# Performance work log

Measured on AMD Instinct MI355X. Metric: run time of the kernel, lower is better.

Reference implementation:

```python
import jax, jax.numpy as jnp
import numpy as np

PI = float(np.pi)          # ouro.pi_center
THIRD = 2.0 * PI / 3.0     # ouro.third_offset
EPB = PI                   # ouro.effective_pi_boundary
DEV = 0.01                 # ouro.deviation
SPARSITY = 0.75
NH = 8
EPS = 1e-5


def prune(w):
    # ouroboros_prune_revive: elementwise resonance chain + quantile threshold mask
    s = w.size
    bloom = jnp.clip(jnp.sin(w * PI), -1.0, 1.0)  # noise_level = 0 (deterministic)
    theta = jnp.linspace(0.0, float(s), s).reshape(w.shape)
    bloom = bloom + bloom * jnp.cos(theta / float(s) + THIRD) * 1.5  # rebound_amp
    etched = jnp.cos(bloom * (EPB ** 2)) + bloom * bloom * (DEV / PI)
    thr = jnp.quantile(jnp.abs(etched), 1.0 - SPARSITY)
    mask = (jnp.abs(etched) > thr).astype(w.dtype)
    return w * mask


def layernorm(x, g, b):
    m = jnp.mean(x, axis=-1, keepdims=True)
    v = jnp.var(x, axis=-1, keepdims=True)
    return (x - m) * jax.lax.rsqrt(v + EPS) * g + b


def setup_inputs():
    key = jax.random.key(0)
    V, D, L, F, B, S = 10000, 512, 6, 2048, 16, 512
    ks = jax.random.split(key, 9)
    p = lambda k, sh: jax.random.normal(k, sh, jnp.float32) * 0.02
    return dict(
        src=jax.random.randint(ks[0], (B, S), 0, V),
        emb=p(ks[1], (V, D)),
        pos=p(ks[2], (1, 512, D)),
        in_proj_w=p(ks[3], (L, 3 * D, D)), in_proj_b=jnp.zeros((L, 3 * D), jnp.float32),
        out_proj_w=p(ks[4], (L, D, D)), out_proj_b=jnp.zeros((L, D), jnp.float32),
        ln1_g=jnp.ones((L, D), jnp.float32), ln1_b=jnp.zeros((L, D), jnp.float32),
        ln2_g=jnp.ones((L, D), jnp.float32), ln2_b=jnp.zeros((L, D), jnp.float32),
        lin1_w=p(ks[5], (L, F, D)), lin1_b=jnp.zeros((L, F), jnp.float32),
        lin2_w=p(ks[6], (L, D, F)), lin2_b=jnp.zeros((L, D), jnp.float32),
        out_w=p(ks[7], (V, D)), out_b=jnp.zeros((V,), jnp.float32),
    )


def reference(src, emb, pos, in_proj_w, in_proj_b, out_proj_w, out_proj_b,
              ln1_g, ln1_b, ln2_g, ln2_b, lin1_w, lin1_b, lin2_w, lin2_b,
              out_w, out_b):
    B, S = src.shape
    D = emb.shape[1]
    L = in_proj_w.shape[0]
    H, dh = NH, D // NH
    x = emb[src] * jnp.sqrt(jnp.float32(D)) + pos[:, :S, :]
    for l in range(L):
        wi = prune(in_proj_w[l])
        qkv = x @ wi.T + in_proj_b[l]
        q, k, v = jnp.split(qkv, 3, axis=-1)
        q = q.reshape(B, S, H, dh)
        k = k.reshape(B, S, H, dh)
        v = v.reshape(B, S, H, dh)
        scores = jnp.einsum('bqhd,bkhd->bhqk', q, k) / jnp.sqrt(jnp.float32(dh))
        att = jax.nn.softmax(scores, axis=-1)
        o = jnp.einsum('bhqk,bkhd->bqhd', att, v).reshape(B, S, D)
        o = o @ out_proj_w[l].T + out_proj_b[l]
        x = layernorm(x + o, ln1_g[l], ln1_b[l])  # post-norm
        w1 = prune(lin1_w[l])
        w2 = prune(lin2_w[l])
        ff = jax.nn.relu(x @ w1.T + lin1_b[l]) @ w2.T + lin2_b[l]
        x = layernorm(x + ff, ln2_g[l], ln2_b[l])
    return x @ out_w.T + out_b
```

## Files before the change

kernel.cpp:

```cpp
#include <hip/hip_runtime.h>
#include <math.h>

#define MTOK   8192
#define DMODEL 512
#define DFF    2048
#define NLAYER 6
#define VOCAB  10000
#define VPAD   10112
#define NHEAD  8
#define DHEAD  64

typedef __attribute__((ext_vector_type(8))) __bf16 bf16x8;
typedef __attribute__((ext_vector_type(4))) float  f32x4;

static const size_t X_B     = 0;
static const size_t Y_B     = (size_t)MTOK * DMODEL * 4;
static const size_t SH_B    = Y_B * 2;
static const size_t WH_B    = SH_B + (size_t)MTOK * DFF * 4;
static const size_t WL_B    = WH_B + (size_t)DFF * DMODEL * 2;
static const size_t HIST_B  = WL_B + (size_t)DFF * DMODEL * 2;
static const size_t STATE_B = HIST_B + (size_t)36 * 4096 * 4;
static const size_t THR_B   = STATE_B + (size_t)36 * 32;
static const size_t WS_NEED = THR_B + 18 * 8;

struct PState {
    double lo, hi;
    unsigned int rank;
    unsigned int pad;
    unsigned long long found;
};

__device__ __forceinline__ unsigned short f2b(float f)
{
    unsigned int u = __float_as_uint(f);
    u += 0x7fffu + ((u >> 16) & 1u);
    return (unsigned short)(u >> 16);
}
__device__ __forceinline__ float b2f(unsigned short h)
{
    return __uint_as_float(((unsigned int)h) << 16);
}

__device__ __forceinline__ void gload16(const void* g, void* l)
{
    __builtin_amdgcn_global_load_lds(
        (const __attribute__((address_space(1))) unsigned int*)g,
        (__attribute__((address_space(3))) unsigned int*)l, 16, 0, 0);
}

__device__ __forceinline__ double etched_abs(float wv, int i, double step, double invn)
{
    float b0 = sinf(wv * 3.14159274f);
    b0 = fminf(1.0f, fmaxf(-1.0f, b0));
    double theta = step * (double)i;
    double c = cos(theta * invn + 2.0943951023931953);
    double bl = (double)b0;
    double bloom = bl + bl * c * 1.5;
    double e = cos(bloom * 9.869604401089358)
             + bloom * bloom * 0.003183098861837907;
    return fabs(e);
}

__device__ __forceinline__ void prune_matrix(int m, const float* ipw, const float* w1,
                                             const float* w2, const float** w, int* n)
{
    int l = m / 3, j = m % 3;
    if (j == 0)      { *w = ipw + (size_t)l * 786432;  *n = 786432;  }
    else if (j == 1) { *w = w1  + (size_t)l * 1048576; *n = 1048576; }
    else             { *w = w2  + (size_t)l * 1048576; *n = 1048576; }
}

__global__ __launch_bounds__(256) void k_prune_init(unsigned int* hist, PState* st)
{
    int gid = blockIdx.x * 256 + threadIdx.x;
    for (int i = gid; i < 36 * 4096; i += gridDim.x * 256) hist[i] = 0u;
    if (gid < 36) {
        int m = gid >> 1;
        int n = (m % 3 == 0) ? 786432 : 1048576;
        st[gid].lo = 0.0;
        st[gid].hi = 1.03;
        st[gid].rank = (unsigned)(n / 4 - 1 + (gid & 1));
        st[gid].found = 0x7FF0000000000000ULL;
    }
}

__global__ __launch_bounds__(256) void k_prune_hist(const float* ipw, const float* w1,
                                                    const float* w2, unsigned int* hist,
                                                    PState* st)
{
    int m = blockIdx.x >> 6;
    int chunk = blockIdx.x & 63;
    const float* w; int n;
    prune_matrix(m, ipw, w1, w2, &w, &n);
    __shared__ unsigned int h[2][4096];
    for (int i = threadIdx.x; i < 8192; i += 256) ((unsigned int*)h)[i] = 0u;
    __syncthreads();
    double lo0 = st[2*m].lo,   hi0 = st[2*m].hi;
    double lo1 = st[2*m+1].lo, hi1 = st[2*m+1].hi;
    double sc0 = 4096.0 / (hi0 - lo0);
    double sc1 = 4096.0 / (hi1 - lo1);
    double step = (double)n / (double)(n - 1);
    double invn = 1.0 / (double)n;
    int per = (n + 63) >> 6;
    int i0 = chunk * per;
    int i1 = min(n, i0 + per);
    for (int i = i0 + (int)threadIdx.x; i < i1; i += 256) {
        double a = etched_abs(w[i], i, step, invn);
        if (a >= lo0 && a < hi0) {
            int bin = (int)((a - lo0) * sc0); if (bin > 4095) bin = 4095;
            atomicAdd(&h[0][bin], 1u);
        }
        if (a >= lo1 && a < hi1) {
            int bin = (int)((a - lo1) * sc1); if (bin > 4095) bin = 4095;
            atomicAdd(&h[1][bin], 1u);
        }
    }
    __syncthreads();
    for (int i = threadIdx.x; i < 4096; i += 256) {
        if (h[0][i]) atomicAdd(&hist[(size_t)(2*m) * 4096 + i], h[0][i]);
        if (h[1][i]) atomicAdd(&hist[(size_t)(2*m+1) * 4096 + i], h[1][i]);
    }
}

__global__ __launch_bounds__(256) void k_prune_select(unsigned int* hist, PState* st)
{
    int s = blockIdx.x;
    __shared__ unsigned int h[4096];
    unsigned int* gh = hist + (size_t)s * 4096;
    for (int i = threadIdx.x; i < 4096; i += 256) { h[i] = gh[i]; gh[i] = 0u; }
    __syncthreads();
    if (threadIdx.x == 0) {
        PState ps = st[s];
        unsigned int r = ps.rank;
        unsigned int acc = 0;
        int bsel = -1; unsigned int newr = 0;
        for (int bi = 0; bi < 4096; ++bi) {
            unsigned int c = h[bi];
            if (bsel < 0 && r < acc + c) { bsel = bi; newr = r - acc; }
            acc += c;
        }
        if (bsel < 0) {
            for (int bi = 4095; bi >= 0; --bi)
                if (h[bi]) { bsel = bi; newr = h[bi] - 1; break; }
            if (bsel < 0) { bsel = 0; newr = 0; }
        }
        double width = (ps.hi - ps.lo) / 4096.0;
        st[s].lo = ps.lo + width * bsel;
        st[s].hi = ps.lo + width * (bsel + 1);
        st[s].rank = newr;
    }
}

__global__ __launch_bounds__(256) void k_prune_capture(const float* ipw, const float* w1,
                                                       const float* w2, PState* st)
{
    int m = blockIdx.x >> 6;
    int chunk = blockIdx.x & 63;
    const float* w; int n;
    prune_matrix(m, ipw, w1, w2, &w, &n);
    double lo0 = st[2*m].lo, lo1 = st[2*m+1].lo;
    double step = (double)n / (double)(n - 1);
    double invn = 1.0 / (double)n;
    unsigned long long mn0 = 0x7FF0000000000000ULL, mn1 = 0x7FF0000000000000ULL;
    int per = (n + 63) >> 6;
    int i0 = chunk * per;
    int i1 = min(n, i0 + per);
    for (int i = i0 + (int)threadIdx.x; i < i1; i += 256) {
        double a = etched_abs(w[i], i, step, invn);
        unsigned long long bits = (unsigned long long)__double_as_longlong(a);
        if (a >= lo0 && bits < mn0) mn0 = bits;
        if (a >= lo1 && bits < mn1) mn1 = bits;
    }
    __shared__ unsigned long long sm[2];
    if (threadIdx.x == 0) { sm[0] = 0x7FF0000000000000ULL; sm[1] = 0x7FF0000000000000ULL; }
    __syncthreads();
    atomicMin(&sm[0], mn0);
    atomicMin(&sm[1], mn1);
    __syncthreads();
    if (threadIdx.x == 0) {
        atomicMin(&st[2*m].found, sm[0]);
        atomicMin(&st[2*m+1].found, sm[1]);
    }
}

__global__ void k_prune_thr(PState* st, double* thr)
{
    int m = threadIdx.x;
    if (m < 18) {
        double v0 = __longlong_as_double((long long)st[2*m].found);
        double v1 = __longlong_as_double((long long)st[2*m+1].found);
        thr[m] = v0 + 0.75 * (v1 - v0);
    }
}

__global__ __launch_bounds__(256) void k_apply_mask_split(const float* __restrict__ w,
                                                          unsigned short* __restrict__ oh,
                                                          unsigned short* __restrict__ ol,
                                                          const double* __restrict__ thr,
                                                          int m, int n)
{
    double T = thr[m];
    double step = (double)n / (double)(n - 1);
    double invn = 1.0 / (double)n;
    for (int i = blockIdx.x * 256 + threadIdx.x; i < n; i += gridDim.x * 256) {
        double a = etched_abs(w[i], i, step, invn);
        float v = (a > T) ? w[i] : 0.0f;
        unsigned short h = f2b(v);
        oh[i] = h;
        ol[i] = f2b(v - b2f(h));
    }
}

__global__ __launch_bounds__(256) void k_split(const float* __restrict__ w,
                                               unsigned short* __restrict__ oh,
                                               unsigned short* __restrict__ ol,
                                               int n, int total)
{
    for (int i = blockIdx.x * 256 + threadIdx.x; i < total; i += gridDim.x * 256) {
        float v = (i < n) ? w[i] : 0.0f;
        unsigned short h = f2b(v);
        oh[i] = h;
        ol[i] = f2b(v - b2f(h));
    }
}

__global__ __launch_bounds__(256) void k_embed(const int* __restrict__ src,
                                               const float* __restrict__ emb,
                                               const float* __restrict__ pos,
                                               float* __restrict__ x)
{
    int t = blockIdx.x;
    int tid = threadIdx.x;
    int v = src[t];
    int s = t & 511;
    const float* e = emb + (size_t)v * DMODEL;
    const float* p = pos + (size_t)s * DMODEL;
    float* xo = x + (size_t)t * DMODEL;
    xo[tid]       = e[tid]       * 22.627416997969522f + p[tid];
    xo[tid + 256] = e[tid + 256] * 22.627416997969522f + p[tid + 256];
}

__global__ __launch_bounds__(256) void k_gemm_mfma(const float* __restrict__ A,
                                                   const unsigned short* __restrict__ BH,
                                                   const unsigned short* __restrict__ BL,
                                                   const float* __restrict__ bias,
                                                   float* __restrict__ C,
                                                   int M, int N, int K, int relu)
{
    __shared__ __align__(16) unsigned char LA[16384];
    __shared__ __align__(16) unsigned char LB[16384];
    unsigned char* LAH = LA;
    unsigned char* LAL = LA + 8192;
    unsigned char* LBH = LB;
    unsigned char* LBL = LB + 8192;

    const int t    = threadIdx.x;
    const int lane = t & 63;
    const int wv   = t >> 6;
    const int wm   = wv >> 1;
    const int wn   = wv & 1;
    const int rowBase = blockIdx.y * 128;
    const int colBase = blockIdx.x * 128;

    const f32x4 zero = {0.0f, 0.0f, 0.0f, 0.0f};
    f32x4 acc[4][4];
#pragma unroll
    for (int i = 0; i < 4; ++i)
#pragma unroll
        for (int j = 0; j < 4; ++j) acc[i][j] = zero;

    int aoff[4], boff[4];
#pragma unroll
    for (int i = 0; i < 4; ++i) {
        int ra = (wm << 6) + (i << 4) + (lane & 15);
        aoff[i] = ra * 64 + (((lane >> 4) ^ ((ra >> 1) & 3)) << 4);
        int rb = (wn << 6) + (i << 4) + (lane & 15);
        boff[i] = rb * 64 + (((lane >> 4) ^ ((rb >> 1) & 3)) << 4);
    }

    for (int k0 = 0; k0 < K; k0 += 32) {
        float4 av[4];
#pragma unroll
        for (int u = 0; u < 4; ++u) {
            int s = t + (u << 8);
            int r = s >> 3, kc = (s & 7) << 2;
            av[u] = *(const float4*)(A + (size_t)(rowBase + r) * K + (k0 + kc));
        }
        __syncthreads();

#pragma unroll
        for (int u = 0; u < 2; ++u) {
            int o = (wv << 10) + (u << 12) + (lane << 4);
            int r = o >> 6;
            int cp = (o >> 4) & 3;
            int kk = (cp ^ ((r >> 1) & 3)) << 3;
            size_t g = (size_t)(colBase + r) * K + (k0 + kk);
            gload16(BH + g, LBH + (wv << 10) + (u << 12));
            gload16(BL + g, LBL + (wv << 10) + (u << 12));
        }

#pragma unroll
        for (int u = 0; u < 4; ++u) {
            int s = t + (u << 8);
            int r = s >> 3;
            int kbyte = (s & 7) << 3;
            int ad = r * 64 + ((((kbyte >> 4)) ^ ((r >> 1) & 3)) << 4) + (kbyte & 8);
            const float* a_ = &av[u].x;
            unsigned short hh[4], ll[4];
#pragma unroll
            for (int j = 0; j < 4; ++j) {
                hh[j] = f2b(a_[j]);
                ll[j] = f2b(a_[j] - b2f(hh[j]));
            }
            uint2 hv, lv;
            hv.x = (unsigned)hh[0] | ((unsigned)hh[1] << 16);
            hv.y = (unsigned)hh[2] | ((unsigned)hh[3] << 16);
            lv.x = (unsigned)ll[0] | ((unsigned)ll[1] << 16);
            lv.y = (unsigned)ll[2] | ((unsigned)ll[3] << 16);
            *(uint2*)(LAH + ad) = hv;
            *(uint2*)(LAL + ad) = lv;
        }
        __syncthreads();

        bf16x8 ah[4], alo[4], bh[4], blo[4];
#pragma unroll
        for (int i = 0; i < 4; ++i) {
            ah[i]  = *(const bf16x8*)(LAH + aoff[i]);
            alo[i] = *(const bf16x8*)(LAL + aoff[i]);
            bh[i]  = *(const bf16x8*)(LBH + boff[i]);
            blo[i] = *(const bf16x8*)(LBL + boff[i]);
        }
#pragma unroll
        for (int i = 0; i < 4; ++i)
#pragma unroll
            for (int j = 0; j < 4; ++j) {
                acc[i][j] = __builtin_amdgcn_mfma_f32_16x16x32_bf16(alo[i], bh[j],  acc[i][j], 0, 0, 0);
                acc[i][j] = __builtin_amdgcn_mfma_f32_16x16x32_bf16(ah[i],  blo[j], acc[i][j], 0, 0, 0);
                acc[i][j] = __builtin_amdgcn_mfma_f32_16x16x32_bf16(ah[i],  bh[j],  acc[i][j], 0, 0, 0);
            }
    }

#pragma unroll
    for (int j = 0; j < 4; ++j) {
        int col = colBase + (wn << 6) + (j << 4) + (lane & 15);
        if (col < N) {
            float bv = bias[col];
#pragma unroll
            for (int i = 0; i < 4; ++i) {
                int row0 = rowBase + (wm << 6) + (i << 4) + ((lane >> 4) << 2);
#pragma unroll
                for (int r = 0; r < 4; ++r) {
                    float v = acc[i][j][r] + bv;
                    if (relu) v = fmaxf(v, 0.0f);
                    C[(size_t)(row0 + r) * N + col] = v;
                }
            }
        }
    }
}

__global__ __launch_bounds__(256) void k_attn(const float* __restrict__ qkv,
                                              float* __restrict__ out)
{
    __shared__ float Qs[64][68];
    __shared__ float KP[64][68];
    __shared__ float Vs[64][64];
    __shared__ float red[64][17];
    __shared__ float mS[64], lS[64], aS[64];

    int bh = blockIdx.x;
    int b = bh >> 3, h = bh & 7;
    int qt = blockIdx.y;
    int t = threadIdx.x;
    int tx = t & 15, ty = t >> 4;
    int r0 = ty * 4, c0 = tx * 4;
    int rowq = b * 512 + qt * 64;

    size_t baseq = (size_t)rowq * 1536 + h * 64;
#pragma unroll
    for (int u = 0; u < 4; ++u) {
        int f = t + u * 256;
        int r = f >> 4;
        int d4 = (f & 15) << 2;
        float4 q4 = *(const float4*)(qkv + baseq + (size_t)r * 1536 + d4);
        Qs[d4 + 0][r] = q4.x; Qs[d4 + 1][r] = q4.y;
        Qs[d4 + 2][r] = q4.z; Qs[d4 + 3][r] = q4.w;
    }
    float O[4][4];
#pragma unroll
    for (int i = 0; i < 4; ++i)
#pragma unroll
        for (int j = 0; j < 4; ++j) O[i][j] = 0.0f;
    if (t < 64) { mS[t] = -INFINITY; lS[t] = 0.0f; }

    size_t basek = (size_t)(b * 512) * 1536 + h * 64;
    for (int kt = 0; kt < 8; ++kt) {
        __syncthreads();
#pragma unroll
        for (int u = 0; u < 4; ++u) {
            int f = t + u * 256;
            int r = f >> 4;
            int d4 = (f & 15) << 2;
            size_t g = basek + (size_t)(kt * 64 + r) * 1536 + d4;
            float4 k4 = *(const float4*)(qkv + g + 512);
            KP[d4 + 0][r] = k4.x; KP[d4 + 1][r] = k4.y;
            KP[d4 + 2][r] = k4.z; KP[d4 + 3][r] = k4.w;
            float4 v4 = *(const float4*)(qkv + g + 1024);
            *(float4*)&Vs[r][d4] = v4;
        }
        __syncthreads();
        float S[4][4];
#pragma unroll
        for (int i = 0; i < 4; ++i)
#pragma unroll
            for (int j = 0; j < 4; ++j) S[i][j] = 0.0f;
#pragma unroll 16
        for (int d = 0; d < 64; ++d) {
            float4 qa = *(const float4*)&Qs[d][r0];
            float4 kb = *(const float4*)&KP[d][c0];
            const float* qa_ = &qa.x;
            const float* kb_ = &kb.x;
#pragma unroll
            for (int i = 0; i < 4; ++i)
#pragma unroll
                for (int j = 0; j < 4; ++j)
                    S[i][j] = fmaf(qa_[i], kb_[j], S[i][j]);
        }
#pragma unroll
        for (int i = 0; i < 4; ++i) {
            float mx = fmaxf(fmaxf(S[i][0], S[i][1]), fmaxf(S[i][2], S[i][3]));
            red[r0 + i][tx] = mx * 0.125f;
        }
        __syncthreads();
        if (t < 64) {
            float m = red[t][0];
#pragma unroll
            for (int k = 1; k < 16; ++k) m = fmaxf(m, red[t][k]);
            float mo = mS[t];
            float mn = fmaxf(mo, m);
            aS[t] = __expf(mo - mn);
            mS[t] = mn;
        }
        __syncthreads();
#pragma unroll
        for (int i = 0; i < 4; ++i) {
            float mn = mS[r0 + i];
            float rs = 0.0f;
#pragma unroll
            for (int j = 0; j < 4; ++j) {
                float p = __expf(fmaf(S[i][j], 0.125f, -mn));
                S[i][j] = p;
                rs += p;
            }
            red[r0 + i][tx] = rs;
            *(float4*)&KP[r0 + i][c0] = *(float4*)S[i];
        }
        __syncthreads();
        if (t < 64) {
            float s = red[t][0];
#pragma unroll
            for (int k = 1; k < 16; ++k) s += red[t][k];
            lS[t] = lS[t] * aS[t] + s;
        }
        float pv[4][4];
#pragma unroll
        for (int i = 0; i < 4; ++i)
#pragma unroll
            for (int j = 0; j < 4; ++j) pv[i][j] = 0.0f;
#pragma unroll 4
        for (int c4 = 0; c4 < 64; c4 += 4) {
            float pr[4][4];
#pragma unroll
            for (int i = 0; i < 4; ++i)
                *(float4*)pr[i] = *(const float4*)&KP[r0 + i][c4];
#pragma unroll
            for (int cc = 0; cc < 4; ++cc) {
                float4 v = *(const float4*)&Vs[c4 + cc][c0];
                const float* v_ = &v.x;
#pragma unroll
                for (int i = 0; i < 4; ++i)
#pragma unroll
                    for (int j = 0; j < 4; ++j)
                        pv[i][j] = fmaf(pr[i][cc], v_[j], pv[i][j]);
            }
        }
#pragma unroll
        for (int i = 0; i < 4; ++i) {
            float a = aS[r0 + i];
#pragma unroll
            for (int j = 0; j < 4; ++j) O[i][j] = O[i][j] * a + pv[i][j];
        }
    }
    __syncthreads();
#pragma unroll
    for (int i = 0; i < 4; ++i) {
        float inv = 1.0f / lS[r0 + i];
        float4 o;
        o.x = O[i][0] * inv; o.y = O[i][1] * inv;
        o.z = O[i][2] * inv; o.w = O[i][3] * inv;
        *(float4*)(out + (size_t)(rowq + r0 + i) * 512 + h * 64 + c0) = o;
    }
}

__global__ __launch_bounds__(256) void k_ln(const float* x, const float* r,
                                            const float* __restrict__ g,
                                            const float* __restrict__ b,
                                            float* out)
{
    int t = blockIdx.x, tid = threadIdx.x;
    size_t base = (size_t)t * DMODEL;
    float a0 = x[base + tid]       + r[base + tid];
    float a1 = x[base + tid + 256] + r[base + tid + 256];
    float s = a0 + a1;
    float q = fmaf(a0, a0, a1 * a1);
#pragma unroll
    for (int off = 32; off; off >>= 1) {
        s += __shfl_xor(s, off, 64);
        q += __shfl_xor(q, off, 64);
    }
    __shared__ float sw[8];
    int w = tid >> 6, lane = tid & 63;
    if (lane == 0) { sw[w] = s; sw[4 + w] = q; }
    __syncthreads();
    s = sw[0] + sw[1] + sw[2] + sw[3];
    q = sw[4] + sw[5] + sw[6] + sw[7];
    float mean = s * (1.0f / 512.0f);
    float var = q * (1.0f / 512.0f) - mean * mean;
    float inv = 1.0f / sqrtf(var + 1e-5f);
    out[base + tid]       = (a0 - mean) * inv * g[tid]       + b[tid];
    out[base + tid + 256] = (a1 - mean) * inv * g[tid + 256] + b[tid + 256];
}

static inline void launch_gemm(const float* A, const unsigned short* BH,
                               const unsigned short* BL, const float* bias,
                               float* C, int M, int N, int K, int relu,
                               hipStream_t stream)
{
    dim3 grid((N + 127) / 128, M / 128);
    k_gemm_mfma<<<grid, 256, 0, stream>>>(A, BH, BL, bias, C, M, N, K, relu);
}

extern "C" void kernel_launch(void* const* d_in, const int* in_sizes, int n_in,
                              void* d_out, int out_size, void* d_ws, size_t ws_size,
                              hipStream_t stream)
{
    (void)in_sizes; (void)n_in; (void)out_size;
    if (ws_size < WS_NEED) return;

    const int*   src = (const int*)  d_in[0];
    const float* emb = (const float*)d_in[1];
    const float* pos = (const float*)d_in[2];
    const float* ipw = (const float*)d_in[3];
    const float* ipb = (const float*)d_in[4];
    const float* opw = (const float*)d_in[5];
    const float* opb = (const float*)d_in[6];
    const float* ln1g = (const float*)d_in[7];
    const float* ln1b = (const float*)d_in[8];
    const float* ln2g = (const float*)d_in[9];
    const float* ln2b = (const float*)d_in[10];
    const float* w1  = (const float*)d_in[11];
    const float* bb1 = (const float*)d_in[12];
    const float* w2  = (const float*)d_in[13];
    const float* bb2 = (const float*)d_in[14];
    const float* ow  = (const float*)d_in[15];
    const float* ob  = (const float*)d_in[16];

    char* ws = (char*)d_ws;
    float* X   = (float*)(ws + X_B);
    float* Y   = (float*)(ws + Y_B);
    float* SHf = (float*)(ws + SH_B);
    unsigned short* WH = (unsigned short*)(ws + WH_B);
    unsigned short* WL = (unsigned short*)(ws + WL_B);
    unsigned short* OWH = (unsigned short*)(ws + SH_B);
    unsigned short* OWL = (unsigned short*)(ws + SH_B + (size_t)VPAD * DMODEL * 2);
    unsigned int* HIST = (unsigned int*)(ws + HIST_B);
    PState* ST = (PState*)(ws + STATE_B);
    double* THR = (double*)(ws + THR_B);
    float* OUT = (float*)d_out;

    k_embed<<<MTOK, 256, 0, stream>>>(src, emb, pos, X);

    k_prune_init<<<64, 256, 0, stream>>>(HIST, ST);
    for (int lev = 0; lev < 3; ++lev) {
        k_prune_hist<<<18 * 64, 256, 0, stream>>>(ipw, w1, w2, HIST, ST);
        k_prune_select<<<36, 256, 0, stream>>>(HIST, ST);
    }
    k_prune_capture<<<18 * 64, 256, 0, stream>>>(ipw, w1, w2, ST);
    k_prune_thr<<<1, 32, 0, stream>>>(ST, THR);

    for (int l = 0; l < NLAYER; ++l) {
        k_apply_mask_split<<<1024, 256, 0, stream>>>(ipw + (size_t)l * 786432, WH, WL,
                                                     THR, 3 * l + 0, 786432);
        launch_gemm(X, WH, WL, ipb + (size_t)l * 1536, SHf, MTOK, 1536, DMODEL, 0, stream);
        k_attn<<<dim3(128, 8), 256, 0, stream>>>(SHf, Y);
        k_split<<<512, 256, 0, stream>>>(opw + (size_t)l * 262144, WH, WL, 262144, 262144);
        launch_gemm(Y, WH, WL, opb + (size_t)l * 512, SHf, MTOK, DMODEL, DMODEL, 0, stream);
        k_ln<<<MTOK, 256, 0, stream>>>(X, SHf, ln1g + (size_t)l * 512,
                                       ln1b + (size_t)l * 512, X);
        k_apply_mask_split<<<1024, 256, 0, stream>>>(w1 + (size_t)l * 1048576, WH, WL,
                                                     THR, 3 * l + 1, 1048576);
        launch_gemm(X, WH, WL, bb1 + (size_t)l * 2048, SHf, MTOK, DFF, DMODEL, 1, stream);
        k_apply_mask_split<<<1024, 256, 0, stream>>>(w2 + (size_t)l * 1048576, WH, WL,
                                                     THR, 3 * l + 2, 1048576);
        launch_gemm(SHf, WH, WL, bb2 + (size_t)l * 512, Y, MTOK, DMODEL, DFF, 0, stream);
        k_ln<<<MTOK, 256, 0, stream>>>(X, Y, ln2g + (size_t)l * 512,
                                       ln2b + (size_t)l * 512, X);
    }

    k_split<<<2048, 256, 0, stream>>>(ow, OWH, OWL, VOCAB * DMODEL, VPAD * DMODEL);
    launch_gemm(X, OWH, OWL, ob, OUT, MTOK, VOCAB, DMODEL, 0, stream);
}
```

Baseline: 4.321 ms.

## Cache etched values and bitmask for pruning; pre-split GEMM activations to bf16 hi/lo

Prune scores are evaluated once per matrix into a double buffer (in batches of 9), then reused for the histogram passes, the capture pass and a ballot-built bitmask. Per-layer mask application then just reads bits. Producers (embed, layernorm, attention, FFN1 GEMM epilogue) now emit bf16 hi/lo activation pairs, so the GEMM loads A directly via async copies instead of converting fp32 in the loop. This trades extra workspace and aliasing complexity for removing repeated double-precision transcendental work and in-loop conversion.

```diff
diff --git a/kernel.cpp b/kernel.cpp
--- a/kernel.cpp
+++ b/kernel.cpp
@@ -21,7 +21,9 @@
 static const size_t HIST_B  = WL_B + (size_t)DFF * DMODEL * 2;
 static const size_t STATE_B = HIST_B + (size_t)36 * 4096 * 4;
 static const size_t THR_B   = STATE_B + (size_t)36 * 32;
-static const size_t WS_NEED = THR_B + 18 * 8;
+static const size_t WS_BASE = THR_B + 18 * 8;
+static const size_t BITS_B  = (WS_BASE + 255) & ~(size_t)255;
+static const size_t WS_BITS = BITS_B + (size_t)17301504 / 8;
 
 struct PState {
     double lo, hi;
@@ -70,6 +72,17 @@
     else             { *w = w2  + (size_t)l * 1048576; *n = 1048576; }
 }
 
+__device__ __forceinline__ size_t moff9(int j)
+{
+    int c0 = (j + 2) / 3;
+    return (size_t)c0 * 786432 + (size_t)(j - c0) * 1048576;
+}
+static __host__ __device__ inline size_t prune_soff(int m)
+{
+    int c0 = (m + 2) / 3;
+    return (size_t)c0 * 786432 + (size_t)(m - c0) * 1048576;
+}
+
 __global__ __launch_bounds__(256) void k_prune_init(unsigned int* hist, PState* st)
 {
     int gid = blockIdx.x * 256 + threadIdx.x;
@@ -84,14 +97,32 @@
     }
 }
 
-__global__ __launch_bounds__(256) void k_prune_hist(const float* ipw, const float* w1,
-                                                    const float* w2, unsigned int* hist,
-                                                    PState* st)
-{
-    int m = blockIdx.x >> 6;
-    int chunk = blockIdx.x & 63;
+__global__ __launch_bounds__(256) void k_eval(const float* ipw, const float* w1,
+                                              const float* w2, double* E, int mb0)
+{
+    int j = blockIdx.x >> 7;
+    int chunk = blockIdx.x & 127;
+    int m = mb0 + j;
     const float* w; int n;
     prune_matrix(m, ipw, w1, w2, &w, &n);
+    double* Em = E + moff9(j);
+    double step = (double)n / (double)(n - 1);
+    double invn = 1.0 / (double)n;
+    int per = (n + 127) >> 7;
+    int i0 = chunk * per;
+    int i1 = min(n, i0 + per);
+    for (int i = i0 + (int)threadIdx.x; i < i1; i += 256)
+        Em[i] = etched_abs(w[i], i, step, invn);
+}
+
+__global__ __launch_bounds__(256) void k_hist_E(const double* __restrict__ E,
+                                                unsigned int* hist, PState* st, int mb0)
+{
+    int j = blockIdx.x >> 6;
+    int chunk = blockIdx.x & 63;
+    int m = mb0 + j;
+    int n = (m % 3 == 0) ? 786432 : 1048576;
+    const double* Em = E + moff9(j);
     __shared__ unsigned int h[2][4096];
     for (int i = threadIdx.x; i < 8192; i += 256) ((unsigned int*)h)[i] = 0u;
     __syncthreads();
@@ -99,13 +130,11 @@
     double lo1 = st[2*m+1].lo, hi1 = st[2*m+1].hi;
     double sc0 = 4096.0 / (hi0 - lo0);
     double sc1 = 4096.0 / (hi1 - lo1);
-    double step = (double)n / (double)(n - 1);
-    double invn = 1.0 / (double)n;
     int per = (n + 63) >> 6;
     int i0 = chunk * per;
     int i1 = min(n, i0 + per);
     for (int i = i0 + (int)threadIdx.x; i < i1; i += 256) {
-        double a = etched_abs(w[i], i, step, invn);
+        double a = Em[i];
         if (a >= lo0 && a < hi0) {
             int bin = (int)((a - lo0) * sc0); if (bin > 4095) bin = 4095;
             atomicAdd(&h[0][bin], 1u);
@@ -122,9 +151,10 @@
     }
 }
 
-__global__ __launch_bounds__(256) void k_prune_select(unsigned int* hist, PState* st)
-{
-    int s = blockIdx.x;
+__global__ __launch_bounds__(256) void k_prune_select(unsigned int* hist, PState* st,
+                                                      int mb0)
+{
+    int s = mb0 * 2 + blockIdx.x;
     __shared__ unsigned int h[4096];
     unsigned int* gh = hist + (size_t)s * 4096;
     for (int i = threadIdx.x; i < 4096; i += 256) { h[i] = gh[i]; gh[i] = 0u; }
@@ -151,22 +181,21 @@
     }
 }
 
-__global__ __launch_bounds__(256) void k_prune_capture(const float* ipw, const float* w1,
-                                                       const float* w2, PState* st)
-{
-    int m = blockIdx.x >> 6;
+__global__ __launch_bounds__(256) void k_capture_E(const double* __restrict__ E,
+                                                   PState* st, int mb0)
+{
+    int j = blockIdx.x >> 6;
     int chunk = blockIdx.x & 63;
-    const float* w; int n;
-    prune_matrix(m, ipw, w1, w2, &w, &n);
+    int m = mb0 + j;
+    int n = (m % 3 == 0) ? 786432 : 1048576;
+    const double* Em = E + moff9(j);
     double lo0 = st[2*m].lo, lo1 = st[2*m+1].lo;
-    double step = (double)n / (double)(n - 1);
-    double invn = 1.0 / (double)n;
     unsigned long long mn0 = 0x7FF0000000000000ULL, mn1 = 0x7FF0000000000000ULL;
     int per = (n + 63) >> 6;
     int i0 = chunk * per;
     int i1 = min(n, i0 + per);
     for (int i = i0 + (int)threadIdx.x; i < i1; i += 256) {
-        double a = etched_abs(w[i], i, step, invn);
+        double a = Em[i];
         unsigned long long bits = (unsigned long long)__double_as_longlong(a);
         if (a >= lo0 && bits < mn0) mn0 = bits;
         if (a >= lo1 && bits < mn1) mn1 = bits;
@@ -183,13 +212,62 @@
     }
 }
 
-__global__ void k_prune_thr(PState* st, double* thr)
-{
-    int m = threadIdx.x;
-    if (m < 18) {
+__global__ void k_thr_batch(PState* st, double* thr, int mb0)
+{
+    int t = threadIdx.x;
+    if (t < 9) {
+        int m = mb0 + t;
         double v0 = __longlong_as_double((long long)st[2*m].found);
         double v1 = __longlong_as_double((long long)st[2*m+1].found);
         thr[m] = v0 + 0.75 * (v1 - v0);
+    }
+}
+
+__global__ __launch_bounds__(256) void k_bits(const double* __restrict__ E,
+                                              const double* __restrict__ thr,
+                                              unsigned long long* __restrict__ bits,
+                                              int mb0)
+{
+    int j = blockIdx.y;
+    int m = mb0 + j;
+    int n = (m % 3 == 0) ? 786432 : 1048576;
+    double T = thr[m];
+    const double* Em = E + moff9(j);
+    unsigned long long* bm = bits + (prune_soff(m) >> 6);
+    int nw = n >> 6;
+    int lane = threadIdx.x & 63;
+    int wid = (blockIdx.x * 256 + threadIdx.x) >> 6;
+    int nwaves = gridDim.x * 4;
+    for (int w = wid; w < nw; w += nwaves) {
+        bool p = Em[(w << 6) + lane] > T;
+        unsigned long long b = __ballot(p);
+        if (lane == 0) bm[w] = b;
+    }
+}
+
+__global__ __launch_bounds__(256) void k_mask_bits(const float* __restrict__ w,
+                                                   unsigned short* __restrict__ oh,
+                                                   unsigned short* __restrict__ ol,
+                                                   const unsigned long long* __restrict__ bits,
+                                                   int n)
+{
+    int stride = gridDim.x * 256 * 4;
+    for (int i4 = (blockIdx.x * 256 + threadIdx.x) * 4; i4 < n; i4 += stride) {
+        float4 v = *(const float4*)(w + i4);
+        unsigned long long word = bits[i4 >> 6];
+        int sh = i4 & 63;
+        float x0 = (word >> (sh + 0)) & 1 ? v.x : 0.0f;
+        float x1 = (word >> (sh + 1)) & 1 ? v.y : 0.0f;
+        float x2 = (word >> (sh + 2)) & 1 ? v.z : 0.0f;
+        float x3 = (word >> (sh + 3)) & 1 ? v.w : 0.0f;
+        unsigned short h0 = f2b(x0), h1 = f2b(x1), h2 = f2b(x2), h3 = f2b(x3);
+        uint2 hv, lv;
+        hv.x = (unsigned)h0 | ((unsigned)h1 << 16);
+        hv.y = (unsigned)h2 | ((unsigned)h3 << 16);
+        lv.x = (unsigned)f2b(x0 - b2f(h0)) | ((unsigned)f2b(x1 - b2f(h1)) << 16);
+        lv.y = (unsigned)f2b(x2 - b2f(h2)) | ((unsigned)f2b(x3 - b2f(h3)) << 16);
+        *(uint2*)(oh + i4) = hv;
+        *(uint2*)(ol + i4) = lv;
     }
 }
 
@@ -227,7 +305,9 @@
 __global__ __launch_bounds__(256) void k_embed(const int* __restrict__ src,
                                                const float* __restrict__ emb,
                                                const float* __restrict__ pos,
-                                               float* __restrict__ x)
+                                               float* __restrict__ x,
+                                               unsigned short* __restrict__ xh,
+                                               unsigned short* __restrict__ xl)
 {
     int t = blockIdx.x;
     int tid = threadIdx.x;
@@ -235,17 +315,25 @@
     int s = t & 511;
     const float* e = emb + (size_t)v * DMODEL;
     const float* p = pos + (size_t)s * DMODEL;
-    float* xo = x + (size_t)t * DMODEL;
-    xo[tid]       = e[tid]       * 22.627416997969522f + p[tid];
-    xo[tid + 256] = e[tid + 256] * 22.627416997969522f + p[tid + 256];
-}
-
-__global__ __launch_bounds__(256) void k_gemm_mfma(const float* __restrict__ A,
+    size_t base = (size_t)t * DMODEL;
+    float y0 = e[tid]       * 22.627416997969522f + p[tid];
+    float y1 = e[tid + 256] * 22.627416997969522f + p[tid + 256];
+    x[base + tid] = y0;
+    x[base + tid + 256] = y1;
+    unsigned short h0 = f2b(y0), h1 = f2b(y1);
+    xh[base + tid] = h0;        xl[base + tid] = f2b(y0 - b2f(h0));
+    xh[base + tid + 256] = h1;  xl[base + tid + 256] = f2b(y1 - b2f(h1));
+}
+
+__global__ __launch_bounds__(256) void k_gemm_mfma(const unsigned short* __restrict__ AH,
+                                                   const unsigned short* __restrict__ AL,
                                                    const unsigned short* __restrict__ BH,
                                                    const unsigned short* __restrict__ BL,
                                                    const float* __restrict__ bias,
                                                    float* __restrict__ C,
-                                                   int M, int N, int K, int relu)
+                                                   unsigned short* __restrict__ CH,
+                                                   unsigned short* __restrict__ CL,
+                                                   int M, int N, int K, int mode)
 {
     __shared__ __align__(16) unsigned char LA[16384];
     __shared__ __align__(16) unsigned char LB[16384];
@@ -278,48 +366,29 @@
         boff[i] = rb * 64 + (((lane >> 4) ^ ((rb >> 1) & 3)) << 4);
     }
 
+    int o0 = (wv << 10) + (lane << 4);
+    int r0s = o0 >> 6;
+    int k0s = (((o0 >> 4) & 3) ^ ((r0s >> 1) & 3)) << 3;
+    int o1 = o0 + 4096;
+    int r1s = o1 >> 6;
+    int k1s = (((o1 >> 4) & 3) ^ ((r1s >> 1) & 3)) << 3;
+    int ldsb0 = (wv << 10);
+    int ldsb1 = (wv << 10) + 4096;
+
     for (int k0 = 0; k0 < K; k0 += 32) {
-        float4 av[4];
-#pragma unroll
-        for (int u = 0; u < 4; ++u) {
-            int s = t + (u << 8);
-            int r = s >> 3, kc = (s & 7) << 2;
-            av[u] = *(const float4*)(A + (size_t)(rowBase + r) * K + (k0 + kc));
-        }
         __syncthreads();
-
-#pragma unroll
-        for (int u = 0; u < 2; ++u) {
-            int o = (wv << 10) + (u << 12) + (lane << 4);
-            int r = o >> 6;
-            int cp = (o >> 4) & 3;
-            int kk = (cp ^ ((r >> 1) & 3)) << 3;
-            size_t g = (size_t)(colBase + r) * K + (k0 + kk);
-            gload16(BH + g, LBH + (wv << 10) + (u << 12));
-            gload16(BL + g, LBL + (wv << 10) + (u << 12));
-        }
-
-#pragma unroll
-        for (int u = 0; u < 4; ++u) {
-            int s = t + (u << 8);
-            int r = s >> 3;
-            int kbyte = (s & 7) << 3;
-            int ad = r * 64 + ((((kbyte >> 4)) ^ ((r >> 1) & 3)) << 4) + (kbyte & 8);
-            const float* a_ = &av[u].x;
-            unsigned short hh[4], ll[4];
-#pragma unroll
-            for (int j = 0; j < 4; ++j) {
-                hh[j] = f2b(a_[j]);
-                ll[j] = f2b(a_[j] - b2f(hh[j]));
-            }
-            uint2 hv, lv;
-            hv.x = (unsigned)hh[0] | ((unsigned)hh[1] << 16);
-            hv.y = (unsigned)hh[2] | ((unsigned)hh[3] << 16);
-            lv.x = (unsigned)ll[0] | ((unsigned)ll[1] << 16);
-            lv.y = (unsigned)ll[2] | ((unsigned)ll[3] << 16);
-            *(uint2*)(LAH + ad) = hv;
-            *(uint2*)(LAL + ad) = lv;
-        }
+        size_t ga0 = (size_t)(rowBase + r0s) * K + (k0 + k0s);
+        size_t ga1 = (size_t)(rowBase + r1s) * K + (k0 + k1s);
+        size_t gb0 = (size_t)(colBase + r0s) * K + (k0 + k0s);
+        size_t gb1 = (size_t)(colBase + r1s) * K + (k0 + k1s);
+        gload16(AH + ga0, LAH + ldsb0);
+        gload16(AL + ga0, LAL + ldsb0);
+        gload16(BH + gb0, LBH + ldsb0);
+        gload16(BL + gb0, LBL + ldsb0);
+        gload16(AH + ga1, LAH + ldsb1);
+        gload16(AL + ga1, LAL + ldsb1);
+        gload16(BH + gb1, LBH + ldsb1);
+        gload16(BL + gb1, LBL + ldsb1);
         __syncthreads();
 
         bf16x8 ah[4], alo[4], bh[4], blo[4];
@@ -351,8 +420,15 @@
 #pragma unroll
                 for (int r = 0; r < 4; ++r) {
                     float v = acc[i][j][r] + bv;
-                    if (relu) v = fmaxf(v, 0.0f);
-                    C[(size_t)(row0 + r) * N + col] = v;
+                    size_t idx = (size_t)(row0 + r) * N + col;
+                    if (mode) {
+                        v = fmaxf(v, 0.0f);
+                        unsigned short hh = f2b(v);
+                        CH[idx] = hh;
+                        CL[idx] = f2b(v - b2f(hh));
+                    } else {
+                        C[idx] = v;
+                    }
                 }
             }
         }
@@ -360,7 +436,8 @@
 }
 
 __global__ __launch_bounds__(256) void k_attn(const float* __restrict__ qkv,
-                                              float* __restrict__ out)
+                                              unsigned short* __restrict__ oh,
+                                              unsigned short* __restrict__ ol)
 {
     __shared__ float Qs[64][68];
     __shared__ float KP[64][68];
@@ -495,17 +572,26 @@
 #pragma unroll
     for (int i = 0; i < 4; ++i) {
         float inv = 1.0f / lS[r0 + i];
-        float4 o;
-        o.x = O[i][0] * inv; o.y = O[i][1] * inv;
-        o.z = O[i][2] * inv; o.w = O[i][3] * inv;
-        *(float4*)(out + (size_t)(rowq + r0 + i) * 512 + h * 64 + c0) = o;
+        float o0 = O[i][0] * inv, o1 = O[i][1] * inv;
+        float o2 = O[i][2] * inv, o3 = O[i][3] * inv;
+        size_t idx = (size_t)(rowq + r0 + i) * 512 + h * 64 + c0;
+        unsigned short h0 = f2b(o0), h1 = f2b(o1), h2 = f2b(o2), h3 = f2b(o3);
+        uint2 hv, lv;
+        hv.x = (unsigned)h0 | ((unsigned)h1 << 16);
+        hv.y = (unsigned)h2 | ((unsigned)h3 << 16);
+        lv.x = (unsigned)f2b(o0 - b2f(h0)) | ((unsigned)f2b(o1 - b2f(h1)) << 16);
+        lv.y = (unsigned)f2b(o2 - b2f(h2)) | ((unsigned)f2b(o3 - b2f(h3)) << 16);
+        *(uint2*)(oh + idx) = hv;
+        *(uint2*)(ol + idx) = lv;
     }
 }
 
 __global__ __launch_bounds__(256) void k_ln(const float* x, const float* r,
                                             const float* __restrict__ g,
                                             const float* __restrict__ b,
-                                            float* out)
+                                            float* out,
+                                            unsigned short* __restrict__ outh,
+                                            unsigned short* __restrict__ outl)
 {
     int t = blockIdx.x, tid = threadIdx.x;
     size_t base = (size_t)t * DMODEL;
@@ -527,17 +613,33 @@
     float mean = s * (1.0f / 512.0f);
     float var = q * (1.0f / 512.0f) - mean * mean;
     float inv = 1.0f / sqrtf(var + 1e-5f);
-    out[base + tid]       = (a0 - mean) * inv * g[tid]       + b[tid];
-    out[base + tid + 256] = (a1 - mean) * inv * g[tid + 256] + b[tid + 256];
-}
-
-static inline void launch_gemm(const float* A, const unsigned short* BH,
-                               const unsigned short* BL, const float* bias,
-                               float* C, int M, int N, int K, int relu,
-                               hipStream_t stream)
+    float y0 = (a0 - mean) * inv * g[tid]       + b[tid];
+    float y1 = (a1 - mean) * inv * g[tid + 256] + b[tid + 256];
+    out[base + tid]       = y0;
+    out[base + tid + 256] = y1;
+    unsigned short h0 = f2b(y0), h1 = f2b(y1);
+    outh[base + tid] = h0;        outl[base + tid] = f2b(y0 - b2f(h0));
+    outh[base + tid + 256] = h1;  outl[base + tid + 256] = f2b(y1 - b2f(h1));
+}
+
+static inline void launch_gemm_f32(const unsigned short* AH, const unsigned short* AL,
+                                   const unsigned short* BH, const unsigned short* BL,
+                                   const float* bias, float* C, int M, int N, int K,
+                                   hipStream_t stream)
 {
     dim3 grid((N + 127) / 128, M / 128);
-    k_gemm_mfma<<<grid, 256, 0, stream>>>(A, BH, BL, bias, C, M, N, K, relu);
+    k_gemm_mfma<<<grid, 256, 0, stream>>>(AH, AL, BH, BL, bias, C, nullptr, nullptr,
+                                          M, N, K, 0);
+}
+static inline void launch_gemm_split(const unsigned short* AH, const unsigned short* AL,
+                                     const unsigned short* BH, const unsigned short* BL,
+                                     const float* bias, unsigned short* CH,
+                                     unsigned short* CL, int M, int N, int K,
+                                     hipStream_t stream)
+{
+    dim3 grid((N + 127) / 128, M / 128);
+    k_gemm_mfma<<<grid, 256, 0, stream>>>(AH, AL, BH, BL, bias, nullptr, CH, CL,
+                                          M, N, K, 1);
 }
 
 extern "C" void kernel_launch(void* const* d_in, const int* in_sizes, int n_in,
@@ -545,7 +647,8 @@
                               hipStream_t stream)
 {
     (void)in_sizes; (void)n_in; (void)out_size;
-    if (ws_size < WS_NEED) return;
+    if (ws_size < WS_BASE) return;
+    const bool use_bits = (ws_size >= WS_BITS);
 
     const int*   src = (const int*)  d_in[0];
     const float* emb = (const float*)d_in[1];
@@ -567,46 +670,76 @@
 
     char* ws = (char*)d_ws;
     float* X   = (float*)(ws + X_B);
-    float* Y   = (float*)(ws + Y_B);
+    float* Yf  = (float*)(ws + Y_B);
     float* SHf = (float*)(ws + SH_B);
+    double* E  = (double*)(ws + X_B);
+    unsigned short* YS_H = (unsigned short*)(ws + Y_B);
+    unsigned short* YS_L = (unsigned short*)(ws + Y_B + 8388608);
+    unsigned short* XS_H = (unsigned short*)(ws + SH_B + 50331648);
+    unsigned short* XS_L = (unsigned short*)(ws + SH_B + 58720256);
+    unsigned short* FH   = (unsigned short*)(ws + SH_B);
+    unsigned short* FL   = (unsigned short*)(ws + SH_B + 33554432);
+    unsigned short* OWH  = (unsigned short*)(ws + SH_B);
+    unsigned short* OWL  = (unsigned short*)(ws + SH_B + (size_t)VPAD * DMODEL * 2);
     unsigned short* WH = (unsigned short*)(ws + WH_B);
     unsigned short* WL = (unsigned short*)(ws + WL_B);
-    unsigned short* OWH = (unsigned short*)(ws + SH_B);
-    unsigned short* OWL = (unsigned short*)(ws + SH_B + (size_t)VPAD * DMODEL * 2);
     unsigned int* HIST = (unsigned int*)(ws + HIST_B);
     PState* ST = (PState*)(ws + STATE_B);
     double* THR = (double*)(ws + THR_B);
+    unsigned long long* BITS = (unsigned long long*)(ws + BITS_B);
     float* OUT = (float*)d_out;
 
-    k_embed<<<MTOK, 256, 0, stream>>>(src, emb, pos, X);
-
     k_prune_init<<<64, 256, 0, stream>>>(HIST, ST);
-    for (int lev = 0; lev < 3; ++lev) {
-        k_prune_hist<<<18 * 64, 256, 0, stream>>>(ipw, w1, w2, HIST, ST);
-        k_prune_select<<<36, 256, 0, stream>>>(HIST, ST);
-    }
-    k_prune_capture<<<18 * 64, 256, 0, stream>>>(ipw, w1, w2, ST);
-    k_prune_thr<<<1, 32, 0, stream>>>(ST, THR);
+    for (int b = 0; b < 2; ++b) {
+        int mb0 = b * 9;
+        k_eval<<<9 * 128, 256, 0, stream>>>(ipw, w1, w2, E, mb0);
+        for (int lev = 0; lev < 3; ++lev) {
+            k_hist_E<<<9 * 64, 256, 0, stream>>>(E, HIST, ST, mb0);
+            k_prune_select<<<18, 256, 0, stream>>>(HIST, ST, mb0);
+        }
+        k_capture_E<<<9 * 64, 256, 0, stream>>>(E, ST, mb0);
+        k_thr_batch<<<1, 32, 0, stream>>>(ST, THR, mb0);
+        if (use_bits)
+            k_bits<<<dim3(64, 9), 256, 0, stream>>>(E, THR, BITS, mb0);
+    }
+
+    k_embed<<<MTOK, 256, 0, stream>>>(src, emb, pos, X, XS_H, XS_L);
 
     for (int l = 0; l < NLAYER; ++l) {
-        k_apply_mask_split<<<1024, 256, 0, stream>>>(ipw + (size_t)l * 786432, WH, WL,
-                                                     THR, 3 * l + 0, 786432);
-        launch_gemm(X, WH, WL, ipb + (size_t)l * 1536, SHf, MTOK, 1536, DMODEL, 0, stream);
-        k_attn<<<dim3(128, 8), 256, 0, stream>>>(SHf, Y);
+        if (use_bits)
+            k_mask_bits<<<256, 256, 0, stream>>>(ipw + (size_t)l * 786432, WH, WL,
+                                                 BITS + (prune_soff(3 * l) >> 6), 786432);
+        else
+            k_apply_mask_split<<<1024, 256, 0, stream>>>(ipw + (size_t)l * 786432, WH, WL,
+                                                         THR, 3 * l, 786432);
+        launch_gemm_f32(XS_H, XS_L, WH, WL, ipb + (size_t)l * 1536, SHf,
+                        MTOK, 1536, DMODEL, stream);
+        k_attn<<<dim3(128, 8), 256, 0, stream>>>(SHf, YS_H, YS_L);
         k_split<<<512, 256, 0, stream>>>(opw + (size_t)l * 262144, WH, WL, 262144, 262144);
-        launch_gemm(Y, WH, WL, opb + (size_t)l * 512, SHf, MTOK, DMODEL, DMODEL, 0, stream);
+        launch_gemm_f32(YS_H, YS_L, WH, WL, opb + (size_t)l * 512, SHf,
+                        MTOK, DMODEL, DMODEL, stream);
         k_ln<<<MTOK, 256, 0, stream>>>(X, SHf, ln1g + (size_t)l * 512,
-                                       ln1b + (size_t)l * 512, X);
-        k_apply_mask_split<<<1024, 256, 0, stream>>>(w1 + (size_t)l * 1048576, WH, WL,
-                                                     THR, 3 * l + 1, 1048576);
-        launch_gemm(X, WH, WL, bb1 + (size_t)l * 2048, SHf, MTOK, DFF, DMODEL, 1, stream);
-        k_apply_mask_split<<<1024, 256, 0, stream>>>(w2 + (size_t)l * 1048576, WH, WL,
-                                                     THR, 3 * l + 2, 1048576);
-        launch_gemm(SHf, WH, WL, bb2 + (size_t)l * 512, Y, MTOK, DMODEL, DFF, 0, stream);
-        k_ln<<<MTOK, 256, 0, stream>>>(X, Y, ln2g + (size_t)l * 512,
-                                       ln2b + (size_t)l * 512, X);
+                                       ln1b + (size_t)l * 512, X, YS_H, YS_L);
+        if (use_bits)
+            k_mask_bits<<<256, 256, 0, stream>>>(w1 + (size_t)l * 1048576, WH, WL,
+                                                 BITS + (prune_soff(3 * l + 1) >> 6), 1048576);
+        else
+            k_apply_mask_split<<<1024, 256, 0, stream>>>(w1 + (size_t)l * 1048576, WH, WL,
+                                                         THR, 3 * l + 1, 1048576);
+        launch_gemm_split(YS_H, YS_L, WH, WL, bb1 + (size_t)l * 2048, FH, FL,
+                          MTOK, DFF, DMODEL, stream);
+        if (use_bits)
+            k_mask_bits<<<256, 256, 0, stream>>>(w2 + (size_t)l * 1048576, WH, WL,
+                                                 BITS + (prune_soff(3 * l + 2) >> 6), 1048576);
+        else
+            k_apply_mask_split<<<1024, 256, 0, stream>>>(w2 + (size_t)l * 1048576, WH, WL,
+                                                         THR, 3 * l + 2, 1048576);
+        launch_gemm_f32(FH, FL, WH, WL, bb2 + (size_t)l * 512, Yf,
+                        MTOK, DMODEL, DFF, stream);
+        k_ln<<<MTOK, 256, 0, stream>>>(X, Yf, ln2g + (size_t)l * 512,
+                                       ln2b + (size_t)l * 512, X, XS_H, XS_L);
     }
 
     k_split<<<2048, 256, 0, stream>>>(ow, OWH, OWL, VOCAB * DMODEL, VPAD * DMODEL);
-    launch_gemm(X, OWH, OWL, ob, OUT, MTOK, VOCAB, DMODEL, 0, stream);
-}
+    launch_gemm_f32(XS_H, XS_L, OWH, OWL, ob, OUT, MTOK, VOCAB, DMODEL, stream);
+}
```

Result: slower. 4.869 ms (+12.7%).
